# Optimization experiments

Measured on AMD Instinct MI355X. Metric: run time of the kernel, lower is better.

## Reference

```python
import jax, jax.numpy as jnp
import numpy as np

S, B, D, H, E, K, FF = 1024, 8, 768, 12, 8, 2, 3072


def _ln(x, w, b, eps=1e-5):
    m = x.mean(-1, keepdims=True)
    v = ((x - m) ** 2).mean(-1, keepdims=True)
    return (x - m) / jnp.sqrt(v + eps) * w + b


def setup_inputs() -> dict:
    key = jax.random.key(0)
    ks = jax.random.split(key, 12)
    s = 0.02
    return {
        "x": jax.random.normal(ks[0], (S, B, D), dtype=jnp.float32),
        "ln1_w": jnp.ones((D,), jnp.float32),
        "ln1_b": jnp.zeros((D,), jnp.float32),
        "in_proj_w": jax.random.normal(ks[1], (3 * D, D), jnp.float32) * s,
        "in_proj_b": jnp.zeros((3 * D,), jnp.float32),
        "out_proj_w": jax.random.normal(ks[2], (D, D), jnp.float32) * s,
        "out_proj_b": jnp.zeros((D,), jnp.float32),
        "ln2_w": jnp.ones((D,), jnp.float32),
        "ln2_b": jnp.zeros((D,), jnp.float32),
        "gate_w": jax.random.normal(ks[3], (E, D), jnp.float32) * s,
        "w1": jax.random.normal(ks[4], (E, D, FF), jnp.float32) * s,
        "b1": jnp.zeros((E, FF), jnp.float32),
        "w2": jax.random.normal(ks[5], (E, FF, D), jnp.float32) * s,
        "b2": jnp.zeros((E, D), jnp.float32),
    }


def reference(x, ln1_w, ln1_b, in_proj_w, in_proj_b, out_proj_w, out_proj_b,
              ln2_w, ln2_b, gate_w, w1, b1, w2, b2):
    s, b, d = x.shape
    hd = d // H
    # --- self attention (nn.MultiheadAttention, seq-first, no mask) ---
    h = _ln(x, ln1_w, ln1_b)
    qkv = h @ in_proj_w.T + in_proj_b            # [S, B, 3D]
    q, k, v = jnp.split(qkv, 3, axis=-1)

    def heads(t):
        return t.reshape(s, b, H, hd).transpose(1, 2, 0, 3)  # [B, H, S, hd]

    q, k, v = heads(q) * (hd ** -0.5), heads(k), heads(v)
    att = jax.nn.softmax(jnp.einsum('bhqd,bhkd->bhqk', q, k), axis=-1)
    o = jnp.einsum('bhqk,bhkd->bhqd', att, v).transpose(2, 0, 1, 3).reshape(s, b, d)
    o = o @ out_proj_w.T + out_proj_b
    x = x + o
    # --- MoE FFN ---
    h2 = _ln(x, ln2_w, ln2_b)
    tok = h2.reshape(-1, d)                      # [T, D], T = S*B
    logits = tok @ gate_w.T                      # [T, E]
    rw = jax.nn.softmax(logits.astype(jnp.float32), axis=-1)
    rw_top, sel = jax.lax.top_k(rw, K)           # [T, K]
    rw_top = rw_top / rw_top.sum(-1, keepdims=True)
    rw_top = rw_top.astype(tok.dtype)
    out = jnp.zeros_like(tok)
    for e in range(E):  # small fixed expert loop; math matches gather/scatter dispatch
        we = jnp.where(sel == e, rw_top, 0.0).sum(-1)       # [T] combine weight
        mid = tok @ w1[e] + b1[e]
        mid = mid * jax.nn.sigmoid(1.702 * mid)              # QuickGELU
        out = out + we[:, None] * (mid @ w2[e] + b2[e])
    return x + out.reshape(s, b, d), logits
```

## Files before the change

kernel.cpp:

```cpp
#include <hip/hip_runtime.h>
#include <stdint.h>

#define S_LEN  1024
#define BATCH  8
#define DMODEL 768
#define NHEAD  12
#define HDIM   64
#define NEXP   8
#define FFDIM  3072
#define NTOK   8192
#define D3     2304
#define NGATH  16384
#define MAXWL  136

typedef unsigned short u16;
typedef unsigned int   u32;
typedef __attribute__((ext_vector_type(8))) short bf16x8;
typedef __attribute__((ext_vector_type(4))) float f32x4;
typedef __attribute__((ext_vector_type(4))) short s16x4;

__device__ __forceinline__ u16 f2bf(float f){
  u32 x = __float_as_uint(f);
  x += 0x7fffu + ((x >> 16) & 1u);
  return (u16)(x >> 16);
}
__device__ __forceinline__ float bf2f(u16 u){
  return __uint_as_float(((u32)u) << 16);
}
__device__ __forceinline__ u32 pkbf(float a, float b){
  u32 d; asm("v_cvt_pk_bf16_f32 %0, %1, %2" : "=v"(d) : "v"(a), "v"(b)); return d;
}
__device__ __forceinline__ void gl_lds16(const void* g, void* l){
  __builtin_amdgcn_global_load_lds(
      (const __attribute__((address_space(1))) u32*)(uintptr_t)g,
      (__attribute__((address_space(3))) u32*)(u32)(uintptr_t)l,
      16, 0, 0);
}
__device__ __forceinline__ int swz64(int r){ return ((r & 7) ^ ((r >> 3) & 7)) << 4; }

__global__ __launch_bounds__(256)
void cvt_bf16(const float* __restrict__ in, u16* __restrict__ out, int n)
{
  int i = (blockIdx.x * 256 + threadIdx.x) * 4;
  if (i + 3 < n) {
    float4 v = *(const float4*)(in + i);
    out[i]     = f2bf(v.x);
    out[i + 1] = f2bf(v.y);
    out[i + 2] = f2bf(v.z);
    out[i + 3] = f2bf(v.w);
  }
}

__global__ __launch_bounds__(256)
void transpose_cvt(const float* __restrict__ in, u16* __restrict__ out, int rows, int cols)
{
  __shared__ float tile[32][33];
  const size_t eo = (size_t)blockIdx.z * rows * cols;
  in  += eo; out += eo;
  const int bx = blockIdx.x * 32, by = blockIdx.y * 32;
  const int tx = threadIdx.x, ty = threadIdx.y;
  #pragma unroll
  for (int i = 0; i < 4; i++)
    tile[ty + i * 8][tx] = in[(size_t)(by + ty + i * 8) * cols + bx + tx];
  __syncthreads();
  #pragma unroll
  for (int i = 0; i < 4; i++)
    out[(size_t)(bx + ty + i * 8) * rows + by + tx] = f2bf(tile[tx][ty + i * 8]);
}

__global__ __launch_bounds__(256)
void ln_fwd(const float* __restrict__ x, const float* __restrict__ w, const float* __restrict__ b,
            u16* __restrict__ out)
{
  const int t = blockIdx.x, tid = threadIdx.x;
  const float* xr = x + (size_t)t * DMODEL;
  const float v0 = xr[tid], v1 = xr[tid + 256], v2 = xr[tid + 512];
  float s = v0 + v1 + v2, ss = v0 * v0 + v1 * v1 + v2 * v2;
  #pragma unroll
  for (int d = 1; d < 64; d <<= 1) { s += __shfl_xor(s, d); ss += __shfl_xor(ss, d); }
  __shared__ float rs[4], rq[4];
  if ((tid & 63) == 0) { rs[tid >> 6] = s; rq[tid >> 6] = ss; }
  __syncthreads();
  s  = rs[0] + rs[1] + rs[2] + rs[3];
  ss = rq[0] + rq[1] + rq[2] + rq[3];
  const float mean = s * (1.f / DMODEL);
  const float rstd = rsqrtf(ss * (1.f / DMODEL) - mean * mean + 1e-5f);
  u16* orow = out + (size_t)t * DMODEL;
  orow[tid]       = f2bf((v0 - mean) * rstd * w[tid]       + b[tid]);
  orow[tid + 256] = f2bf((v1 - mean) * rstd * w[tid + 256] + b[tid + 256]);
  orow[tid + 512] = f2bf((v2 - mean) * rstd * w[tid + 512] + b[tid + 512]);
}

__global__ __launch_bounds__(256)
void ln2_gate(const float* __restrict__ x1, const float* __restrict__ w, const float* __restrict__ b,
              const float* __restrict__ gate_w, u16* __restrict__ h2,
              float* __restrict__ logits, float* __restrict__ selw, int* __restrict__ seli)
{
  const int t = blockIdx.x, tid = threadIdx.x;
  const float* xr = x1 + (size_t)t * DMODEL;
  const float v0 = xr[tid], v1 = xr[tid + 256], v2 = xr[tid + 512];
  float s = v0 + v1 + v2, ss = v0 * v0 + v1 * v1 + v2 * v2;
  #pragma unroll
  for (int d = 1; d < 64; d <<= 1) { s += __shfl_xor(s, d); ss += __shfl_xor(ss, d); }
  __shared__ float rs[4], rq[4];
  if ((tid & 63) == 0) { rs[tid >> 6] = s; rq[tid >> 6] = ss; }
  __syncthreads();
  s  = rs[0] + rs[1] + rs[2] + rs[3];
  ss = rq[0] + rq[1] + rq[2] + rq[3];
  const float mean = s * (1.f / DMODEL);
  const float rstd = rsqrtf(ss * (1.f / DMODEL) - mean * mean + 1e-5f);
  __shared__ float row[DMODEL];
  const float y0 = (v0 - mean) * rstd * w[tid]       + b[tid];
  const float y1 = (v1 - mean) * rstd * w[tid + 256] + b[tid + 256];
  const float y2 = (v2 - mean) * rstd * w[tid + 512] + b[tid + 512];
  row[tid] = y0; row[tid + 256] = y1; row[tid + 512] = y2;
  u16* hr = h2 + (size_t)t * DMODEL;
  hr[tid] = f2bf(y0); hr[tid + 256] = f2bf(y1); hr[tid + 512] = f2bf(y2);
  __syncthreads();
  __shared__ float lg[NEXP];
  if (tid < 64) {
    const int e = tid >> 3, j = tid & 7;
    const float* gw = gate_w + e * DMODEL;
    float a = 0.f;
    for (int d = j; d < DMODEL; d += 8) a += row[d] * gw[d];
    a += __shfl_xor(a, 1); a += __shfl_xor(a, 2); a += __shfl_xor(a, 4);
    if (j == 0) lg[e] = a;
  }
  __syncthreads();
  if (tid < NEXP) logits[(size_t)t * NEXP + tid] = lg[tid];
  if (tid == 0) {
    int ia = 0, ib = -1;
    float va = -1e30f, vb = -1e30f;
    #pragma unroll
    for (int e = 0; e < NEXP; e++) {
      const float p = lg[e];
      if (p > va)      { vb = va; ib = ia; va = p; ia = e; }
      else if (p > vb) { vb = p; ib = e; }
    }
    const float pb = __expf(vb - va);
    const float inv = 1.f / (1.f + pb);
    selw[2 * t]     = inv;
    selw[2 * t + 1] = pb * inv;
    seli[2 * t]     = ia;
    seli[2 * t + 1] = ib;
  }
}

__global__ __launch_bounds__(256)
void route_count(const int* __restrict__ seli, int* __restrict__ blkcnt)
{
  __shared__ int c[NEXP];
  const int tid = threadIdx.x;
  if (tid < NEXP) c[tid] = 0;
  __syncthreads();
  const int t = blockIdx.x * 256 + tid;
  atomicAdd(&c[seli[2 * t]], 1);
  atomicAdd(&c[seli[2 * t + 1]], 1);
  __syncthreads();
  if (tid < NEXP) blkcnt[blockIdx.x * NEXP + tid] = c[tid];
}

__global__ void route_scan(const int* __restrict__ blkcnt, int* __restrict__ offs,
                           int* __restrict__ blkbase, int* __restrict__ wl, int* __restrict__ nwork)
{
  const int tid = threadIdx.x;
  __shared__ int tot[NEXP];
  __shared__ int off_s[NEXP + 1];
  if (tid < NEXP) {
    int s = 0;
    for (int blk = 0; blk < 32; blk++) s += blkcnt[blk * NEXP + tid];
    tot[tid] = s;
  }
  __syncthreads();
  if (tid == 0) {
    int run = 0;
    for (int e = 0; e < NEXP; e++) { off_s[e] = run; run += tot[e]; }
    off_s[NEXP] = run;
    int nw = 0;
    for (int e = 0; e < NEXP; e++) {
      const int nb = (tot[e] + 127) >> 7;
      for (int i2 = 0; i2 < nb; i2++) wl[nw++] = (e << 16) | i2;
    }
    nwork[0] = nw;
  }
  __syncthreads();
  if (tid <= NEXP) offs[tid] = off_s[tid];
  if (tid < NEXP) {
    int run = off_s[tid];
    for (int blk = 0; blk < 32; blk++) { blkbase[blk * NEXP + tid] = run; run += blkcnt[blk * NEXP + tid]; }
  }
}

__global__ __launch_bounds__(256)
void route_place(const int* __restrict__ seli, const int* __restrict__ blkbase,
                 int* __restrict__ perm, int* __restrict__ posmap)
{
  __shared__ int cnts[2][4][NEXP];
  __shared__ int base[NEXP];
  const int tid = threadIdx.x, l = tid & 63, w = tid >> 6, blk = blockIdx.x;
  const int t = blk * 256 + tid;
  const unsigned long long ltm = (1ull << l) - 1ull;
  int my_e[2], my_r[2];
  my_e[0] = seli[2 * t]; my_e[1] = seli[2 * t + 1];
  my_r[0] = 0; my_r[1] = 0;
  if (tid < NEXP) base[tid] = blkbase[blk * NEXP + tid];
  #pragma unroll
  for (int k = 0; k < 2; k++) {
    #pragma unroll
    for (int ee = 0; ee < NEXP; ee++) {
      const unsigned long long msk = __ballot(my_e[k] == ee);
      if (my_e[k] == ee) my_r[k] = (int)__popcll(msk & ltm);
      if (l == ee) cnts[k][w][ee] = (int)__popcll(msk);
    }
  }
  __syncthreads();
  #pragma unroll
  for (int k = 0; k < 2; k++) {
    const int e = my_e[k];
    int pre = base[e];
    for (int k2 = 0; k2 < 2; k2++)
      for (int w2 = 0; w2 < 4; w2++)
        if (k2 < k || (k2 == k && w2 < w)) pre += cnts[k2][w2][e];
    const int pos = pre + my_r[k];
    perm[pos] = t;
    posmap[2 * t + k] = pos;
  }
}

template<int MODE>
__global__ __launch_bounds__(256)
void gemm128(const u16* __restrict__ A, const u16* __restrict__ Bw,
             int M, int N, int Kd,
             const float* __restrict__ bias, const float* __restrict__ resid,
             void* __restrict__ outp,
             const int* __restrict__ perm, const int* __restrict__ offs,
             const int* __restrict__ wl, const int* __restrict__ nwork)
{
  __shared__ u16 As[2][128 * 64];
  __shared__ u16 Bs[2][128 * 64];
  const int tid = threadIdx.x;
  const int l   = tid & 63;
  const int w   = tid >> 6;
  const int wm  = w >> 1, wn = w & 1;
  const int bn  = blockIdx.y;

  int gbase = 0, cnt = M, e = 0, bm = blockIdx.x;
  if (MODE >= 2) {
    if (blockIdx.x >= nwork[0]) return;
    const int wk = wl[blockIdx.x];
    e  = wk >> 16;
    bm = wk & 0xffff;
    gbase = offs[e];
    cnt   = offs[e + 1] - gbase;
  }
  const u16*   Bp = Bw   + (MODE >= 2 ? (size_t)e * N * Kd : 0);
  const float* bp = bias + (MODE >= 2 ? e * N : 0);

  int arow[4], acol[4], brow[4];
  #pragma unroll
  for (int i = 0; i < 4; i++) {
    const int c = tid + 256 * i;
    const int r = c >> 3;
    const int f = (r & 7) ^ ((r >> 3) & 7);
    acol[i] = ((c & 7) ^ f) * 8;
    brow[i] = bn * 128 + r;
    int g;
    if (MODE == 2)      { int gp = gbase + bm * 128 + r; if (gp > NGATH - 1) gp = NGATH - 1; g = perm[gp]; }
    else if (MODE == 3) { int gp = gbase + bm * 128 + r; if (gp > NGATH - 1) gp = NGATH - 1; g = gp; }
    else                g = bm * 128 + r;
    arow[i] = g;
  }

  f32x4 acc[4][4] = {};
  const int nk = Kd >> 6;

  #pragma unroll
  for (int i = 0; i < 4; i++) {
    gl_lds16(A  + (size_t)arow[i] * Kd + acol[i], &As[0][(i * 256 + w * 64) * 8]);
    gl_lds16(Bp + (size_t)brow[i] * Kd + acol[i], &Bs[0][(i * 256 + w * 64) * 8]);
  }

  int cur = 0;
  for (int kt = 0; kt < nk; kt++) {
    const bool pf = (kt + 1 < nk);
    if (pf) {
      const int kb = (kt + 1) * 64;
      #pragma unroll
      for (int i = 0; i < 4; i++) {
        gl_lds16(A  + (size_t)arow[i] * Kd + kb + acol[i], &As[cur ^ 1][(i * 256 + w * 64) * 8]);
        gl_lds16(Bp + (size_t)brow[i] * Kd + kb + acol[i], &Bs[cur ^ 1][(i * 256 + w * 64) * 8]);
      }
      asm volatile("s_waitcnt vmcnt(8)" ::: "memory");
    } else {
      asm volatile("s_waitcnt vmcnt(0)" ::: "memory");
    }
    __builtin_amdgcn_s_barrier();
    __builtin_amdgcn_sched_barrier(0);

    #pragma unroll
    for (int ks = 0; ks < 2; ks++) {
      bf16x8 af[4], bv[4];
      #pragma unroll
      for (int m = 0; m < 4; m++) {
        const int row = wm * 64 + m * 16 + (l & 15);
        af[m] = *(const bf16x8*)((const char*)&As[cur][0] +
                  ((row * 128 + ks * 64 + (l >> 4) * 16) ^ swz64(row)));
      }
      #pragma unroll
      for (int n = 0; n < 4; n++) {
        const int row = wn * 64 + n * 16 + (l & 15);
        bv[n] = *(const bf16x8*)((const char*)&Bs[cur][0] +
                  ((row * 128 + ks * 64 + (l >> 4) * 16) ^ swz64(row)));
      }
      #pragma unroll
      for (int m = 0; m < 4; m++)
        #pragma unroll
        for (int n = 0; n < 4; n++)
          acc[m][n] = __builtin_amdgcn_mfma_f32_16x16x32_bf16(bv[n], af[m], acc[m][n], 0, 0, 0);
    }
    if (pf) __builtin_amdgcn_s_barrier();
    cur ^= 1;
  }

  f32x4 biasv[4];
  int   c0[4];
  #pragma unroll
  for (int n = 0; n < 4; n++) {
    c0[n] = bn * 128 + wn * 64 + n * 16 + ((l >> 4) << 2);
    biasv[n] = *(const f32x4*)(bp + c0[n]);
  }
  #pragma unroll
  for (int m = 0; m < 4; m++) {
    const int row = bm * 128 + wm * 64 + m * 16 + (l & 15);
    #pragma unroll
    for (int n = 0; n < 4; n++) {
      f32x4 v = acc[m][n] + biasv[n];
      if (MODE == 0) {
        *(uint2*)((u16*)outp + (size_t)row * N + c0[n]) =
            make_uint2(pkbf(v[0], v[1]), pkbf(v[2], v[3]));
      } else if (MODE == 1) {
        const size_t o = (size_t)row * N + c0[n];
        f32x4 rv = *(const f32x4*)(resid + o);
        v += rv;
        *(f32x4*)((float*)outp + o) = v;
      } else if (MODE == 2) {
        if (row < cnt) {
          #pragma unroll
          for (int r = 0; r < 4; r++)
            v[r] = v[r] * __builtin_amdgcn_rcpf(1.f + __expf(-1.702f * v[r]));
          *(uint2*)((u16*)outp + (size_t)(gbase + row) * FFDIM + c0[n]) =
              make_uint2(pkbf(v[0], v[1]), pkbf(v[2], v[3]));
        }
      } else {
        if (row < cnt)
          *(uint2*)((u16*)outp + (size_t)(gbase + row) * DMODEL + c0[n]) =
              make_uint2(pkbf(v[0], v[1]), pkbf(v[2], v[3]));
      }
    }
  }
}

__global__ __launch_bounds__(256)
void attn_fwd(const u16* __restrict__ qkv, u16* __restrict__ o)
{
  __shared__ u16 Ksw[64 * 64];
  __shared__ u16 Vt [64 * 64];
  __shared__ u16 Pl [4 * 16 * 64];
  const int tid = threadIdx.x;
  const int l   = tid & 63, w = tid >> 6;
  const int qt  = blockIdx.x;
  const int b_  = blockIdx.y / NHEAD;
  const int hh  = blockIdx.y % NHEAD;

  const int qrow = qt * 64 + w * 16 + (l & 15);
  const size_t qoff = ((size_t)(qrow * BATCH + b_)) * D3 + hh * HDIM + (l >> 4) * 8;
  const bf16x8 qa0 = *(const bf16x8*)&qkv[qoff];
  const bf16x8 qa1 = *(const bf16x8*)&qkv[qoff + 32];

  f32x4 oacc[4] = {};
  float m_[4], l_[4];
  #pragma unroll
  for (int r = 0; r < 4; r++) { m_[r] = -1e30f; l_[r] = 0.f; }

  u16* Pw = Pl + w * 1024;
  const int pswz = swz64(l & 15);

  for (int kt = 0; kt < 16; kt++) {
    #pragma unroll
    for (int i = 0; i < 2; i++) {
      const int c = tid + 256 * i;
      const int key = c >> 3, dimb = (c & 7) * 8;
      const size_t gb = ((size_t)((kt * 64 + key) * BATCH + b_)) * D3 + hh * HDIM + dimb;
      const bf16x8 kd = *(const bf16x8*)&qkv[gb + DMODEL];
      const bf16x8 vd = *(const bf16x8*)&qkv[gb + 2 * DMODEL];
      *(bf16x8*)((char*)Ksw + ((key * 128 + dimb * 2) ^ swz64(key))) = kd;
      #pragma unroll
      for (int j = 0; j < 8; j++) {
        const int dim = dimb + j;
        *(u16*)((char*)Vt + ((dim * 128 + key * 2) ^ swz64(dim))) = (u16)vd[j];
      }
    }
    __syncthreads();

    f32x4 sc[4] = {};
    #pragma unroll
    for (int kb2 = 0; kb2 < 4; kb2++) {
      const int key = kb2 * 16 + (l & 15);
      const int ksz = swz64(key);
      #pragma unroll
      for (int ks = 0; ks < 2; ks++) {
        const bf16x8 kf = *(const bf16x8*)((char*)Ksw +
            ((key * 128 + (ks * 32 + (l >> 4) * 8) * 2) ^ ksz));
        sc[kb2] = __builtin_amdgcn_mfma_f32_16x16x32_bf16(ks ? qa1 : qa0, kf, sc[kb2], 0, 0, 0);
      }
    }
    #pragma unroll
    for (int kb2 = 0; kb2 < 4; kb2++)
      #pragma unroll
      for (int r = 0; r < 4; r++) sc[kb2][r] *= 0.125f;

    float nm[4], corr[4], ps[4];
    #pragma unroll
    for (int r = 0; r < 4; r++) {
      float pm = fmaxf(fmaxf(sc[0][r], sc[1][r]), fmaxf(sc[2][r], sc[3][r]));
      pm = fmaxf(pm, __shfl_xor(pm, 1));
      pm = fmaxf(pm, __shfl_xor(pm, 2));
      pm = fmaxf(pm, __shfl_xor(pm, 4));
      pm = fmaxf(pm, __shfl_xor(pm, 8));
      nm[r]   = fmaxf(m_[r], pm);
      corr[r] = __expf(m_[r] - nm[r]);
      m_[r]   = nm[r];
      ps[r]   = 0.f;
    }
    #pragma unroll
    for (int kb2 = 0; kb2 < 4; kb2++) {
      #pragma unroll
      for (int r = 0; r < 4; r++) {
        const float p = __expf(sc[kb2][r] - nm[r]);
        ps[r] += p;
        const int prow = (l >> 4) * 4 + r;
        const int pcol = kb2 * 16 + (l & 15);
        *(u16*)((char*)Pw + ((prow * 128 + pcol * 2) ^ swz64(prow))) = f2bf(p);
      }
    }
    #pragma unroll
    for (int r = 0; r < 4; r++) {
      float s = ps[r];
      s += __shfl_xor(s, 1); s += __shfl_xor(s, 2);
      s += __shfl_xor(s, 4); s += __shfl_xor(s, 8);
      l_[r] = l_[r] * corr[r] + s;
      #pragma unroll
      for (int ob = 0; ob < 4; ob++) oacc[ob][r] *= corr[r];
    }

    #pragma unroll
    for (int ob = 0; ob < 4; ob++) {
      const int dim = ob * 16 + (l & 15);
      const int vsz = swz64(dim);
      #pragma unroll
      for (int ks = 0; ks < 2; ks++) {
        const int kko = (ks * 32 + (l >> 4) * 8) * 2;
        const bf16x8 pf = *(const bf16x8*)((char*)Pw + (((l & 15) * 128 + kko) ^ pswz));
        const bf16x8 vf = *(const bf16x8*)((char*)Vt + ((dim * 128 + kko) ^ vsz));
        oacc[ob] = __builtin_amdgcn_mfma_f32_16x16x32_bf16(pf, vf, oacc[ob], 0, 0, 0);
      }
    }
    __syncthreads();
  }

  #pragma unroll
  for (int r = 0; r < 4; r++) {
    const float inv = 1.f / l_[r];
    const int qs = qt * 64 + w * 16 + (l >> 4) * 4 + r;
    #pragma unroll
    for (int ob = 0; ob < 4; ob++)
      o[((size_t)(qs * BATCH + b_)) * DMODEL + hh * HDIM + ob * 16 + (l & 15)] =
          f2bf(oacc[ob][r] * inv);
  }
}

__global__ __launch_bounds__(192)
void moe_combine(const float* __restrict__ x1, const u16* __restrict__ eout,
                 const int* __restrict__ posmap, const float* __restrict__ selw,
                 float* __restrict__ out)
{
  const int t = blockIdx.x, j = threadIdx.x;
  const int p0 = posmap[2 * t], p1 = posmap[2 * t + 1];
  const float w0 = selw[2 * t], w1 = selw[2 * t + 1];
  const float4 xv = ((const float4*)(x1 + (size_t)t * DMODEL))[j];
  const s16x4 a = ((const s16x4*)(eout + (size_t)p0 * DMODEL))[j];
  const s16x4 c = ((const s16x4*)(eout + (size_t)p1 * DMODEL))[j];
  float4 r;
  r.x = xv.x + w0 * bf2f((u16)a[0]) + w1 * bf2f((u16)c[0]);
  r.y = xv.y + w0 * bf2f((u16)a[1]) + w1 * bf2f((u16)c[1]);
  r.z = xv.z + w0 * bf2f((u16)a[2]) + w1 * bf2f((u16)c[2]);
  r.w = xv.w + w0 * bf2f((u16)a[3]) + w1 * bf2f((u16)c[3]);
  ((float4*)(out + (size_t)t * DMODEL))[j] = r;
}

#define MB (1ull << 20)
static const size_t OFF_H    = 0;
static const size_t OFF_QKV  = 16 * MB;
static const size_t OFF_O    = 54 * MB;
static const size_t OFF_IPW  = 67 * MB;
static const size_t OFF_OPW  = 71 * MB;
static const size_t OFF_MID  = 0;
static const size_t OFF_X1   = 101 * MB;
static const size_t OFF_H2   = 127 * MB;
static const size_t OFF_W1T  = 140 * MB;
static const size_t OFF_W2T  = 178 * MB;
static const size_t OFF_EOUT = 216 * MB;
static const size_t OFF_SELW = 242 * MB;
static const size_t OFF_PERM = 242 * MB + (1 << 16);
static const size_t OFF_POS  = 242 * MB + (2 << 16);
static const size_t OFF_SELI = 242 * MB + (3 << 16);
static const size_t OFF_BCNT = 242 * MB + (4 << 16);
static const size_t OFF_BBASE= 242 * MB + (4 << 16) + 4096;
static const size_t OFF_OFFS = 242 * MB + (4 << 16) + 8192;
static const size_t OFF_WL   = 242 * MB + (5 << 16);
static const size_t OFF_NW   = 242 * MB + (5 << 16) + 1024;

extern "C" void kernel_launch(void* const* d_in, const int* in_sizes, int n_in,
                              void* d_out, int out_size, void* d_ws, size_t ws_size,
                              hipStream_t stream)
{
  const float* x     = (const float*)d_in[0];
  const float* ln1w  = (const float*)d_in[1];
  const float* ln1b  = (const float*)d_in[2];
  const float* ipw_f = (const float*)d_in[3];
  const float* ipb   = (const float*)d_in[4];
  const float* opw_f = (const float*)d_in[5];
  const float* opb   = (const float*)d_in[6];
  const float* ln2w  = (const float*)d_in[7];
  const float* ln2b  = (const float*)d_in[8];
  const float* gatew = (const float*)d_in[9];
  const float* w1    = (const float*)d_in[10];
  const float* b1    = (const float*)d_in[11];
  const float* w2    = (const float*)d_in[12];
  const float* b2    = (const float*)d_in[13];

  char* ws = (char*)d_ws;
  u16*   h    = (u16*)(ws + OFF_H);
  u16*   qkv  = (u16*)(ws + OFF_QKV);
  u16*   ob   = (u16*)(ws + OFF_O);
  u16*   ipw  = (u16*)(ws + OFF_IPW);
  u16*   opw  = (u16*)(ws + OFF_OPW);
  u16*   mid  = (u16*)(ws + OFF_MID);
  float* x1   = (float*)(ws + OFF_X1);
  u16*   h2   = (u16*)(ws + OFF_H2);
  u16*   w1t  = (u16*)(ws + OFF_W1T);
  u16*   w2t  = (u16*)(ws + OFF_W2T);
  u16*   eout = (u16*)(ws + OFF_EOUT);
  float* selw = (float*)(ws + OFF_SELW);
  int*   perm = (int*)(ws + OFF_PERM);
  int*   posm = (int*)(ws + OFF_POS);
  int*   seli = (int*)(ws + OFF_SELI);
  int*   bcnt = (int*)(ws + OFF_BCNT);
  int*   bbas = (int*)(ws + OFF_BBASE);
  int*   offs = (int*)(ws + OFF_OFFS);
  int*   wl   = (int*)(ws + OFF_WL);
  int*   nwork= (int*)(ws + OFF_NW);
  float* outx  = (float*)d_out;
  float* outlg = outx + (size_t)NTOK * DMODEL;

  cvt_bf16<<<(D3 * DMODEL) / 1024, 256, 0, stream>>>(ipw_f, ipw, D3 * DMODEL);
  cvt_bf16<<<(DMODEL * DMODEL) / 1024, 256, 0, stream>>>(opw_f, opw, DMODEL * DMODEL);
  transpose_cvt<<<dim3(FFDIM / 32, DMODEL / 32, NEXP), dim3(32, 8), 0, stream>>>(w1, w1t, DMODEL, FFDIM);
  transpose_cvt<<<dim3(DMODEL / 32, FFDIM / 32, NEXP), dim3(32, 8), 0, stream>>>(w2, w2t, FFDIM, DMODEL);

  ln_fwd<<<NTOK, 256, 0, stream>>>(x, ln1w, ln1b, h);
  gemm128<0><<<dim3(NTOK / 128, D3 / 128, 1), 256, 0, stream>>>(
      h, ipw, NTOK, D3, DMODEL, ipb, nullptr, qkv, nullptr, nullptr, nullptr, nullptr);
  attn_fwd<<<dim3(S_LEN / 64, BATCH * NHEAD), 256, 0, stream>>>(qkv, ob);
  gemm128<1><<<dim3(NTOK / 128, DMODEL / 128, 1), 256, 0, stream>>>(
      ob, opw, NTOK, DMODEL, DMODEL, opb, x, x1, nullptr, nullptr, nullptr, nullptr);

  ln2_gate<<<NTOK, 256, 0, stream>>>(x1, ln2w, ln2b, gatew, h2, outlg, selw, seli);
  route_count<<<32, 256, 0, stream>>>(seli, bcnt);
  route_scan<<<1, 64, 0, stream>>>(bcnt, offs, bbas, wl, nwork);
  route_place<<<32, 256, 0, stream>>>(seli, bbas, perm, posm);

  gemm128<2><<<dim3(MAXWL, FFDIM / 128, 1), 256, 0, stream>>>(
      h2, w1t, NGATH, FFDIM, DMODEL, b1, nullptr, mid, perm, offs, wl, nwork);
  gemm128<3><<<dim3(MAXWL, DMODEL / 128, 1), 256, 0, stream>>>(
      mid, w2t, NGATH, DMODEL, FFDIM, b2, nullptr, eout, nullptr, offs, wl, nwork);

  moe_combine<<<NTOK, 192, 0, stream>>>(x1, eout, posm, selw, outx);
}
```

Measured before the change: 546.7 us.

## Use 256x256 GEMM tiles with 512 threads for QKV and MoE expert GEMMs

Adds a gemm256 kernel that uses 8 waves, a 256x256 output tile and 128 KB of dynamic LDS for double-buffered A/B tiles. It replaces the 128x128 kernel for the QKV projection and both MoE expert GEMMs. Routing now builds work items in 256-row chunks to match, and MAXWL is lowered. The out-projection keeps a dedicated 128-tile kernel with the fused residual add. The aim is higher arithmetic intensity per loaded tile and fewer global loads. The costs are more padding waste per expert, coarser wave quantization across CUs (e.g. 288 blocks for QKV, 240 for the second expert GEMM), and only one block resident per CU.

```diff
diff --git a/kernel.cpp b/kernel.cpp
--- a/kernel.cpp
+++ b/kernel.cpp
@@ -11,7 +11,7 @@
 #define NTOK   8192
 #define D3     2304
 #define NGATH  16384
-#define MAXWL  136
+#define MAXWL  80
 
 typedef unsigned short u16;
 typedef unsigned int   u32;
@@ -178,7 +178,7 @@
     off_s[NEXP] = run;
     int nw = 0;
     for (int e = 0; e < NEXP; e++) {
-      const int nb = (tot[e] + 127) >> 7;
+      const int nb = (tot[e] + 255) >> 8;
       for (int i2 = 0; i2 < nb; i2++) wl[nw++] = (e << 16) | i2;
     }
     nwork[0] = nw;
@@ -228,20 +228,19 @@
 }
 
 template<int MODE>
-__global__ __launch_bounds__(256)
-void gemm128(const u16* __restrict__ A, const u16* __restrict__ Bw,
+__global__ __launch_bounds__(512, 2)
+void gemm256(const u16* __restrict__ A, const u16* __restrict__ Bw,
              int M, int N, int Kd,
-             const float* __restrict__ bias, const float* __restrict__ resid,
+             const float* __restrict__ bias,
              void* __restrict__ outp,
              const int* __restrict__ perm, const int* __restrict__ offs,
              const int* __restrict__ wl, const int* __restrict__ nwork)
 {
-  __shared__ u16 As[2][128 * 64];
-  __shared__ u16 Bs[2][128 * 64];
+  extern __shared__ u16 smem[];
   const int tid = threadIdx.x;
   const int l   = tid & 63;
   const int w   = tid >> 6;
-  const int wm  = w >> 1, wn = w & 1;
+  const int wm  = w >> 2, wn = w & 3;
   const int bn  = blockIdx.y;
 
   int gbase = 0, cnt = M, e = 0, bm = blockIdx.x;
@@ -259,25 +258,25 @@
   int arow[4], acol[4], brow[4];
   #pragma unroll
   for (int i = 0; i < 4; i++) {
-    const int c = tid + 256 * i;
+    const int c = tid + 512 * i;
     const int r = c >> 3;
     const int f = (r & 7) ^ ((r >> 3) & 7);
     acol[i] = ((c & 7) ^ f) * 8;
-    brow[i] = bn * 128 + r;
+    brow[i] = bn * 256 + r;
     int g;
-    if (MODE == 2)      { int gp = gbase + bm * 128 + r; if (gp > NGATH - 1) gp = NGATH - 1; g = perm[gp]; }
-    else if (MODE == 3) { int gp = gbase + bm * 128 + r; if (gp > NGATH - 1) gp = NGATH - 1; g = gp; }
-    else                g = bm * 128 + r;
+    if (MODE == 2)      { int gp = gbase + bm * 256 + r; if (gp > NGATH - 1) gp = NGATH - 1; g = perm[gp]; }
+    else if (MODE == 3) { int gp = gbase + bm * 256 + r; if (gp > NGATH - 1) gp = NGATH - 1; g = gp; }
+    else                g = bm * 256 + r;
     arow[i] = g;
   }
 
-  f32x4 acc[4][4] = {};
+  f32x4 acc[8][4] = {};
   const int nk = Kd >> 6;
 
   #pragma unroll
   for (int i = 0; i < 4; i++) {
-    gl_lds16(A  + (size_t)arow[i] * Kd + acol[i], &As[0][(i * 256 + w * 64) * 8]);
-    gl_lds16(Bp + (size_t)brow[i] * Kd + acol[i], &Bs[0][(i * 256 + w * 64) * 8]);
+    gl_lds16(A  + (size_t)arow[i] * Kd + acol[i], &smem[(tid + 512 * i) * 8]);
+    gl_lds16(Bp + (size_t)brow[i] * Kd + acol[i], &smem[32768 + (tid + 512 * i) * 8]);
   }
 
   int cur = 0;
@@ -285,10 +284,12 @@
     const bool pf = (kt + 1 < nk);
     if (pf) {
       const int kb = (kt + 1) * 64;
+      u16* Anx = smem + (cur ^ 1) * 16384;
+      u16* Bnx = smem + 32768 + (cur ^ 1) * 16384;
       #pragma unroll
       for (int i = 0; i < 4; i++) {
-        gl_lds16(A  + (size_t)arow[i] * Kd + kb + acol[i], &As[cur ^ 1][(i * 256 + w * 64) * 8]);
-        gl_lds16(Bp + (size_t)brow[i] * Kd + kb + acol[i], &Bs[cur ^ 1][(i * 256 + w * 64) * 8]);
+        gl_lds16(A  + (size_t)arow[i] * Kd + kb + acol[i], &Anx[(tid + 512 * i) * 8]);
+        gl_lds16(Bp + (size_t)brow[i] * Kd + kb + acol[i], &Bnx[(tid + 512 * i) * 8]);
       }
       asm volatile("s_waitcnt vmcnt(8)" ::: "memory");
     } else {
@@ -297,26 +298,24 @@
     __builtin_amdgcn_s_barrier();
     __builtin_amdgcn_sched_barrier(0);
 
+    const char* Ac = (const char*)(smem + cur * 16384);
+    const char* Bc = (const char*)(smem + 32768 + cur * 16384);
     #pragma unroll
     for (int ks = 0; ks < 2; ks++) {
-      bf16x8 af[4], bv[4];
-      #pragma unroll
-      for (int m = 0; m < 4; m++) {
-        const int row = wm * 64 + m * 16 + (l & 15);
-        af[m] = *(const bf16x8*)((const char*)&As[cur][0] +
-                  ((row * 128 + ks * 64 + (l >> 4) * 16) ^ swz64(row)));
-      }
+      bf16x8 bv[4];
       #pragma unroll
       for (int n = 0; n < 4; n++) {
         const int row = wn * 64 + n * 16 + (l & 15);
-        bv[n] = *(const bf16x8*)((const char*)&Bs[cur][0] +
-                  ((row * 128 + ks * 64 + (l >> 4) * 16) ^ swz64(row)));
-      }
-      #pragma unroll
-      for (int m = 0; m < 4; m++)
+        bv[n] = *(const bf16x8*)(Bc + ((row * 128 + ks * 64 + (l >> 4) * 16) ^ swz64(row)));
+      }
+      #pragma unroll
+      for (int m = 0; m < 8; m++) {
+        const int row = wm * 128 + m * 16 + (l & 15);
+        const bf16x8 af = *(const bf16x8*)(Ac + ((row * 128 + ks * 64 + (l >> 4) * 16) ^ swz64(row)));
         #pragma unroll
         for (int n = 0; n < 4; n++)
-          acc[m][n] = __builtin_amdgcn_mfma_f32_16x16x32_bf16(bv[n], af[m], acc[m][n], 0, 0, 0);
+          acc[m][n] = __builtin_amdgcn_mfma_f32_16x16x32_bf16(bv[n], af, acc[m][n], 0, 0, 0);
+      }
     }
     if (pf) __builtin_amdgcn_s_barrier();
     cur ^= 1;
@@ -326,23 +325,18 @@
   int   c0[4];
   #pragma unroll
   for (int n = 0; n < 4; n++) {
-    c0[n] = bn * 128 + wn * 64 + n * 16 + ((l >> 4) << 2);
+    c0[n] = bn * 256 + wn * 64 + n * 16 + ((l >> 4) << 2);
     biasv[n] = *(const f32x4*)(bp + c0[n]);
   }
   #pragma unroll
-  for (int m = 0; m < 4; m++) {
-    const int row = bm * 128 + wm * 64 + m * 16 + (l & 15);
+  for (int m = 0; m < 8; m++) {
+    const int row = bm * 256 + wm * 128 + m * 16 + (l & 15);
     #pragma unroll
     for (int n = 0; n < 4; n++) {
       f32x4 v = acc[m][n] + biasv[n];
       if (MODE == 0) {
         *(uint2*)((u16*)outp + (size_t)row * N + c0[n]) =
             make_uint2(pkbf(v[0], v[1]), pkbf(v[2], v[3]));
-      } else if (MODE == 1) {
-        const size_t o = (size_t)row * N + c0[n];
-        f32x4 rv = *(const f32x4*)(resid + o);
-        v += rv;
-        *(f32x4*)((float*)outp + o) = v;
       } else if (MODE == 2) {
         if (row < cnt) {
           #pragma unroll
@@ -356,6 +350,98 @@
           *(uint2*)((u16*)outp + (size_t)(gbase + row) * DMODEL + c0[n]) =
               make_uint2(pkbf(v[0], v[1]), pkbf(v[2], v[3]));
       }
+    }
+  }
+}
+
+__global__ __launch_bounds__(256)
+void gemm128_op(const u16* __restrict__ A, const u16* __restrict__ Bw,
+                int M, int N, int Kd,
+                const float* __restrict__ bias, const float* __restrict__ resid,
+                float* __restrict__ outp)
+{
+  __shared__ u16 As[2][128 * 64];
+  __shared__ u16 Bs[2][128 * 64];
+  const int tid = threadIdx.x;
+  const int l   = tid & 63;
+  const int w   = tid >> 6;
+  const int wm  = w >> 1, wn = w & 1;
+  const int bn  = blockIdx.y, bm = blockIdx.x;
+
+  int arow[4], acol[4], brow[4];
+  #pragma unroll
+  for (int i = 0; i < 4; i++) {
+    const int c = tid + 256 * i;
+    const int r = c >> 3;
+    const int f = (r & 7) ^ ((r >> 3) & 7);
+    acol[i] = ((c & 7) ^ f) * 8;
+    brow[i] = bn * 128 + r;
+    arow[i] = bm * 128 + r;
+  }
+
+  f32x4 acc[4][4] = {};
+  const int nk = Kd >> 6;
+  #pragma unroll
+  for (int i = 0; i < 4; i++) {
+    gl_lds16(A  + (size_t)arow[i] * Kd + acol[i], &As[0][(i * 256 + w * 64) * 8]);
+    gl_lds16(Bw + (size_t)brow[i] * Kd + acol[i], &Bs[0][(i * 256 + w * 64) * 8]);
+  }
+  int cur = 0;
+  for (int kt = 0; kt < nk; kt++) {
+    const bool pf = (kt + 1 < nk);
+    if (pf) {
+      const int kb = (kt + 1) * 64;
+      #pragma unroll
+      for (int i = 0; i < 4; i++) {
+        gl_lds16(A  + (size_t)arow[i] * Kd + kb + acol[i], &As[cur ^ 1][(i * 256 + w * 64) * 8]);
+        gl_lds16(Bw + (size_t)brow[i] * Kd + kb + acol[i], &Bs[cur ^ 1][(i * 256 + w * 64) * 8]);
+      }
+      asm volatile("s_waitcnt vmcnt(8)" ::: "memory");
+    } else {
+      asm volatile("s_waitcnt vmcnt(0)" ::: "memory");
+    }
+    __builtin_amdgcn_s_barrier();
+    __builtin_amdgcn_sched_barrier(0);
+    #pragma unroll
+    for (int ks = 0; ks < 2; ks++) {
+      bf16x8 af[4], bv[4];
+      #pragma unroll
+      for (int m = 0; m < 4; m++) {
+        const int row = wm * 64 + m * 16 + (l & 15);
+        af[m] = *(const bf16x8*)((const char*)&As[cur][0] +
+                  ((row * 128 + ks * 64 + (l >> 4) * 16) ^ swz64(row)));
+      }
+      #pragma unroll
+      for (int n = 0; n < 4; n++) {
+        const int row = wn * 64 + n * 16 + (l & 15);
+        bv[n] = *(const bf16x8*)((const char*)&Bs[cur][0] +
+                  ((row * 128 + ks * 64 + (l >> 4) * 16) ^ swz64(row)));
+      }
+      #pragma unroll
+      for (int m = 0; m < 4; m++)
+        #pragma unroll
+        for (int n = 0; n < 4; n++)
+          acc[m][n] = __builtin_amdgcn_mfma_f32_16x16x32_bf16(bv[n], af[m], acc[m][n], 0, 0, 0);
+    }
+    if (pf) __builtin_amdgcn_s_barrier();
+    cur ^= 1;
+  }
+
+  f32x4 biasv[4];
+  int   c0[4];
+  #pragma unroll
+  for (int n = 0; n < 4; n++) {
+    c0[n] = bn * 128 + wn * 64 + n * 16 + ((l >> 4) << 2);
+    biasv[n] = *(const f32x4*)(bias + c0[n]);
+  }
+  #pragma unroll
+  for (int m = 0; m < 4; m++) {
+    const int row = bm * 128 + wm * 64 + m * 16 + (l & 15);
+    #pragma unroll
+    for (int n = 0; n < 4; n++) {
+      const size_t o = (size_t)row * N + c0[n];
+      f32x4 v = acc[m][n] + biasv[n] + *(const f32x4*)(resid + o);
+      *(f32x4*)(outp + o) = v;
     }
   }
 }
@@ -563,27 +649,32 @@
   float* outx  = (float*)d_out;
   float* outlg = outx + (size_t)NTOK * DMODEL;
 
+  static const int LDS_BYTES = 131072;
+  (void)hipFuncSetAttribute((const void*)gemm256<0>, hipFuncAttributeMaxDynamicSharedMemorySize, LDS_BYTES);
+  (void)hipFuncSetAttribute((const void*)gemm256<2>, hipFuncAttributeMaxDynamicSharedMemorySize, LDS_BYTES);
+  (void)hipFuncSetAttribute((const void*)gemm256<3>, hipFuncAttributeMaxDynamicSharedMemorySize, LDS_BYTES);
+
   cvt_bf16<<<(D3 * DMODEL) / 1024, 256, 0, stream>>>(ipw_f, ipw, D3 * DMODEL);
   cvt_bf16<<<(DMODEL * DMODEL) / 1024, 256, 0, stream>>>(opw_f, opw, DMODEL * DMODEL);
   transpose_cvt<<<dim3(FFDIM / 32, DMODEL / 32, NEXP), dim3(32, 8), 0, stream>>>(w1, w1t, DMODEL, FFDIM);
   transpose_cvt<<<dim3(DMODEL / 32, FFDIM / 32, NEXP), dim3(32, 8), 0, stream>>>(w2, w2t, FFDIM, DMODEL);
 
   ln_fwd<<<NTOK, 256, 0, stream>>>(x, ln1w, ln1b, h);
-  gemm128<0><<<dim3(NTOK / 128, D3 / 128, 1), 256, 0, stream>>>(
-      h, ipw, NTOK, D3, DMODEL, ipb, nullptr, qkv, nullptr, nullptr, nullptr, nullptr);
+  gemm256<0><<<dim3(NTOK / 256, D3 / 256, 1), 512, LDS_BYTES, stream>>>(
+      h, ipw, NTOK, D3, DMODEL, ipb, qkv, nullptr, nullptr, nullptr, nullptr);
   attn_fwd<<<dim3(S_LEN / 64, BATCH * NHEAD), 256, 0, stream>>>(qkv, ob);
-  gemm128<1><<<dim3(NTOK / 128, DMODEL / 128, 1), 256, 0, stream>>>(
-      ob, opw, NTOK, DMODEL, DMODEL, opb, x, x1, nullptr, nullptr, nullptr, nullptr);
+  gemm128_op<<<dim3(NTOK / 128, DMODEL / 128, 1), 256, 0, stream>>>(
+      ob, opw, NTOK, DMODEL, DMODEL, opb, x, x1);
 
   ln2_gate<<<NTOK, 256, 0, stream>>>(x1, ln2w, ln2b, gatew, h2, outlg, selw, seli);
   route_count<<<32, 256, 0, stream>>>(seli, bcnt);
   route_scan<<<1, 64, 0, stream>>>(bcnt, offs, bbas, wl, nwork);
   route_place<<<32, 256, 0, stream>>>(seli, bbas, perm, posm);
 
-  gemm128<2><<<dim3(MAXWL, FFDIM / 128, 1), 256, 0, stream>>>(
-      h2, w1t, NGATH, FFDIM, DMODEL, b1, nullptr, mid, perm, offs, wl, nwork);
-  gemm128<3><<<dim3(MAXWL, DMODEL / 128, 1), 256, 0, stream>>>(
-      mid, w2t, NGATH, DMODEL, FFDIM, b2, nullptr, eout, nullptr, offs, wl, nwork);
+  gemm256<2><<<dim3(MAXWL, FFDIM / 256, 1), 512, LDS_BYTES, stream>>>(
+      h2, w1t, NGATH, FFDIM, DMODEL, b1, mid, perm, offs, wl, nwork);
+  gemm256<3><<<dim3(MAXWL, DMODEL / 256, 1), 512, LDS_BYTES, stream>>>(
+      mid, w2t, NGATH, DMODEL, FFDIM, b2, eout, nullptr, offs, wl, nwork);
 
   moe_combine<<<NTOK, 192, 0, stream>>>(x1, eout, posm, selw, outx);
 }
```

New measurement: 559.0 us. +2.2%, slower.

## Remap GEMM and attention blocks per XCD; widen weight transpose tiles

Applied to the files above, without the earlier changes.

Flattens the GEMM and attention grids to 1D and applies an XCD-aware remap so that consecutive logical tiles land on the same XCD, keeping the shared B or K/V tiles in that XCD's L2. In the expert GEMMs the remap uses the dynamic work count, so blocks beyond nwork*N/128 exit early. The weight transpose-convert kernel moves to 64x64 tiles with float4 loads and packed bf16 stores to reduce instruction and memory-transaction overhead. The new tile ordering changes the cache access pattern, and the transpose's column reads from the padded LDS tile may hit bank conflicts.

```diff
diff --git a/kernel.cpp b/kernel.cpp
--- a/kernel.cpp
+++ b/kernel.cpp
@@ -38,6 +38,12 @@
 }
 __device__ __forceinline__ int swz64(int r){ return ((r & 7) ^ ((r >> 3) & 7)) << 4; }
 
+__device__ __forceinline__ int xcd_swz(int orig, int nwg){
+  const int q = nwg >> 3, r = nwg & 7;
+  const int xcd = orig & 7, loc = orig >> 3;
+  return (xcd < r ? xcd * (q + 1) : r * (q + 1) + (xcd - r) * q) + loc;
+}
+
 __global__ __launch_bounds__(256)
 void cvt_bf16(const float* __restrict__ in, u16* __restrict__ out, int n)
 {
@@ -54,18 +60,29 @@
 __global__ __launch_bounds__(256)
 void transpose_cvt(const float* __restrict__ in, u16* __restrict__ out, int rows, int cols)
 {
-  __shared__ float tile[32][33];
+  __shared__ float tile[64][65];
   const size_t eo = (size_t)blockIdx.z * rows * cols;
   in  += eo; out += eo;
-  const int bx = blockIdx.x * 32, by = blockIdx.y * 32;
-  const int tx = threadIdx.x, ty = threadIdx.y;
-  #pragma unroll
-  for (int i = 0; i < 4; i++)
-    tile[ty + i * 8][tx] = in[(size_t)(by + ty + i * 8) * cols + bx + tx];
-  __syncthreads();
-  #pragma unroll
-  for (int i = 0; i < 4; i++)
-    out[(size_t)(bx + ty + i * 8) * rows + by + tx] = f2bf(tile[tx][ty + i * 8]);
+  const int bx = blockIdx.x * 64;
+  const int by = blockIdx.y * 64;
+  const int tid = threadIdx.x;
+  #pragma unroll
+  for (int i = 0; i < 4; i++) {
+    const int c = tid + 256 * i;
+    const int r = c >> 4, c4 = (c & 15) * 4;
+    const float4 v = *(const float4*)(in + (size_t)(by + r) * cols + bx + c4);
+    tile[r][c4] = v.x; tile[r][c4 + 1] = v.y; tile[r][c4 + 2] = v.z; tile[r][c4 + 3] = v.w;
+  }
+  __syncthreads();
+  #pragma unroll
+  for (int i = 0; i < 4; i++) {
+    const int c = tid + 256 * i;
+    const int orow = c >> 4, r4 = (c & 15) * 4;
+    uint2 p;
+    p.x = pkbf(tile[r4][orow],     tile[r4 + 1][orow]);
+    p.y = pkbf(tile[r4 + 2][orow], tile[r4 + 3][orow]);
+    *(uint2*)(out + (size_t)(bx + orow) * rows + by + r4) = p;
+  }
 }
 
 __global__ __launch_bounds__(256)
@@ -242,16 +259,24 @@
   const int l   = tid & 63;
   const int w   = tid >> 6;
   const int wm  = w >> 1, wn = w & 1;
-  const int bn  = blockIdx.y;
-
-  int gbase = 0, cnt = M, e = 0, bm = blockIdx.x;
+
+  int gbase = 0, cnt = M, e = 0, bm, bn;
   if (MODE >= 2) {
-    if (blockIdx.x >= nwork[0]) return;
-    const int wk = wl[blockIdx.x];
+    const int nw  = nwork[0];
+    const int nwg = nw * (N >> 7);
+    if ((int)blockIdx.x >= nwg) return;
+    const int t = xcd_swz(blockIdx.x, nwg);
+    bn = t / nw;
+    const int wk = wl[t - bn * nw];
     e  = wk >> 16;
     bm = wk & 0xffff;
     gbase = offs[e];
     cnt   = offs[e + 1] - gbase;
+  } else {
+    const int nbm = M >> 7;
+    const int t = xcd_swz(blockIdx.x, gridDim.x);
+    bn = t / nbm;
+    bm = t - bn * nbm;
   }
   const u16*   Bp = Bw   + (MODE >= 2 ? (size_t)e * N * Kd : 0);
   const float* bp = bias + (MODE >= 2 ? e * N : 0);
@@ -368,9 +393,11 @@
   __shared__ u16 Pl [4 * 16 * 64];
   const int tid = threadIdx.x;
   const int l   = tid & 63, w = tid >> 6;
-  const int qt  = blockIdx.x;
-  const int b_  = blockIdx.y / NHEAD;
-  const int hh  = blockIdx.y % NHEAD;
+  const int tt  = xcd_swz(blockIdx.x, 16 * BATCH * NHEAD);
+  const int qt  = tt & 15;
+  const int bh  = tt >> 4;
+  const int b_  = bh / NHEAD;
+  const int hh  = bh % NHEAD;
 
   const int qrow = qt * 64 + w * 16 + (l & 15);
   const size_t qoff = ((size_t)(qrow * BATCH + b_)) * D3 + hh * HDIM + (l >> 4) * 8;
@@ -565,14 +592,14 @@
 
   cvt_bf16<<<(D3 * DMODEL) / 1024, 256, 0, stream>>>(ipw_f, ipw, D3 * DMODEL);
   cvt_bf16<<<(DMODEL * DMODEL) / 1024, 256, 0, stream>>>(opw_f, opw, DMODEL * DMODEL);
-  transpose_cvt<<<dim3(FFDIM / 32, DMODEL / 32, NEXP), dim3(32, 8), 0, stream>>>(w1, w1t, DMODEL, FFDIM);
-  transpose_cvt<<<dim3(DMODEL / 32, FFDIM / 32, NEXP), dim3(32, 8), 0, stream>>>(w2, w2t, FFDIM, DMODEL);
+  transpose_cvt<<<dim3(FFDIM / 64, DMODEL / 64, NEXP), 256, 0, stream>>>(w1, w1t, DMODEL, FFDIM);
+  transpose_cvt<<<dim3(DMODEL / 64, FFDIM / 64, NEXP), 256, 0, stream>>>(w2, w2t, FFDIM, DMODEL);
 
   ln_fwd<<<NTOK, 256, 0, stream>>>(x, ln1w, ln1b, h);
-  gemm128<0><<<dim3(NTOK / 128, D3 / 128, 1), 256, 0, stream>>>(
+  gemm128<0><<<(NTOK / 128) * (D3 / 128), 256, 0, stream>>>(
       h, ipw, NTOK, D3, DMODEL, ipb, nullptr, qkv, nullptr, nullptr, nullptr, nullptr);
-  attn_fwd<<<dim3(S_LEN / 64, BATCH * NHEAD), 256, 0, stream>>>(qkv, ob);
-  gemm128<1><<<dim3(NTOK / 128, DMODEL / 128, 1), 256, 0, stream>>>(
+  attn_fwd<<<(S_LEN / 64) * BATCH * NHEAD, 256, 0, stream>>>(qkv, ob);
+  gemm128<1><<<(NTOK / 128) * (DMODEL / 128), 256, 0, stream>>>(
       ob, opw, NTOK, DMODEL, DMODEL, opb, x, x1, nullptr, nullptr, nullptr, nullptr);
 
   ln2_gate<<<NTOK, 256, 0, stream>>>(x1, ln2w, ln2b, gatew, h2, outlg, selw, seli);
@@ -580,9 +607,9 @@
   route_scan<<<1, 64, 0, stream>>>(bcnt, offs, bbas, wl, nwork);
   route_place<<<32, 256, 0, stream>>>(seli, bbas, perm, posm);
 
-  gemm128<2><<<dim3(MAXWL, FFDIM / 128, 1), 256, 0, stream>>>(
+  gemm128<2><<<MAXWL * (FFDIM / 128), 256, 0, stream>>>(
       h2, w1t, NGATH, FFDIM, DMODEL, b1, nullptr, mid, perm, offs, wl, nwork);
-  gemm128<3><<<dim3(MAXWL, DMODEL / 128, 1), 256, 0, stream>>>(
+  gemm128<3><<<MAXWL * (DMODEL / 128), 256, 0, stream>>>(
       mid, w2t, NGATH, DMODEL, FFDIM, b2, nullptr, eout, nullptr, offs, wl, nwork);
 
   moe_combine<<<NTOK, 192, 0, stream>>>(x1, eout, posm, selw, outx);
```

Measured after the change: 540.0 us. Within noise of the previous version (-1.2%).
